# Performance work log

Measured on AMD Instinct MI355X. Metric: run time of the kernel, lower is better.

Reference implementation:

```python
import jax, jax.numpy as jnp
from jax import lax
import numpy as np

B, S, I, H, L = 128, 256, 512, 768, 2  # batch, seq, input, hidden, layers


def _lstm_dir(x_seq, Wx, bx, Wh, bh, h0, c0):
    """Run one LSTM direction over x_seq [B,S,D]. Gate order f,i,g,o (as torch.chunk)."""
    xg = jnp.einsum('bsd,dg->bsg', x_seq, Wx) + bx  # precompute input projections [B,S,4H]

    def step(carry, xg_t):
        h, c = carry
        gates = xg_t + h @ Wh + bh
        f, i, g, o = jnp.split(gates, 4, axis=-1)
        c = jax.nn.sigmoid(f) * c + jax.nn.sigmoid(i) * jnp.tanh(g)
        h = jax.nn.sigmoid(o) * jnp.tanh(c)
        return (h, c), h

    (h, c), hs = lax.scan(step, (h0, c0), jnp.swapaxes(xg, 0, 1))  # scan over time
    return jnp.swapaxes(hs, 0, 1), h, c  # outputs [B,S,H], final h, c


def _mk_params(key, in_dim, hid):
    k1, k2 = jax.random.split(key)
    s_x = 1.0 / np.sqrt(in_dim)
    s_h = 1.0 / np.sqrt(hid)
    Wx = jax.random.uniform(k1, (in_dim, 4 * hid), jnp.float32, -s_x, s_x)
    bx = jnp.zeros((4 * hid,), jnp.float32)
    Wh = jax.random.uniform(k2, (hid, 4 * hid), jnp.float32, -s_h, s_h)
    bh = jnp.zeros((4 * hid,), jnp.float32)
    return Wx, bx, Wh, bh


def setup_inputs() -> dict:
    key = jax.random.key(0)
    ks = jax.random.split(key, 5)
    x = jax.random.normal(ks[0], (B, S, I), jnp.float32)
    out = {'x': x}
    names = [('f0', I), ('f1', H), ('b0', I), ('b1', H)]
    for k, (tag, in_dim) in zip(ks[1:], names):
        Wx, bx, Wh, bh = _mk_params(k, in_dim, H)
        out[f'Wx_{tag}'] = Wx
        out[f'bx_{tag}'] = bx
        out[f'Wh_{tag}'] = Wh
        out[f'bh_{tag}'] = bh
    return out


def reference(x, Wx_f0, bx_f0, Wh_f0, bh_f0, Wx_f1, bx_f1, Wh_f1, bh_f1,
              Wx_b0, bx_b0, Wh_b0, bh_b0, Wx_b1, bx_b1, Wh_b1, bh_b1):
    b = x.shape[0]
    z = jnp.zeros((b, H), x.dtype)
    fwd_params = [(Wx_f0, bx_f0, Wh_f0, bh_f0), (Wx_f1, bx_f1, Wh_f1, bh_f1)]
    bwd_params = [(Wx_b0, bx_b0, Wh_b0, bh_b0), (Wx_b1, bx_b1, Wh_b1, bh_b1)]

    inp_f = x
    inp_b = jnp.flip(x, axis=1)  # backward direction consumes reversed sequence
    h_f, c_f, h_b, c_b = [], [], [], []
    for layer in range(L):
        inp_f, hf, cf = _lstm_dir(inp_f, *fwd_params[layer], z, z)
        h_f.append(hf); c_f.append(cf)
        inp_b, hb, cb = _lstm_dir(inp_b, *bwd_params[layer], z, z)
        h_b.append(hb); c_b.append(cb)

    output = jnp.concatenate([inp_f, jnp.flip(inp_b, axis=1)], axis=-1)  # [B,S,2H]
    h_n = jnp.stack(h_f + h_b, axis=0)  # [2L,B,H], forward layers then backward
    c_n = jnp.stack(c_f + c_b, axis=0)
    return output, h_n, c_n
```

## Files before the change

### kernel.cpp

```cpp
#include <hip/hip_runtime.h>

#define BATCH 128
#define SEQ   256
#define IDIM  512
#define HDIM  768
#define G4    3072
#define BK    32
#define LSTR  72

typedef __bf16 bf16;
typedef __bf16 bf16x8 __attribute__((ext_vector_type(8)));
typedef float  f32x4  __attribute__((ext_vector_type(4)));

__device__ __forceinline__ float sigf(float x){ return 1.f/(1.f + __expf(-x)); }
__device__ __forceinline__ float tanhf_(float x){ return 1.f - 2.f/(1.f + __expf(2.f*x)); }


__global__ void convert_x_k(const float* __restrict__ x, bf16* __restrict__ xb){
  long i = ((long)blockIdx.x*256 + threadIdx.x)*8;
  float4 a = *(const float4*)(x+i);
  float4 b = *(const float4*)(x+i+4);
  bf16x8 o;
  o[0]=(bf16)a.x; o[1]=(bf16)a.y; o[2]=(bf16)a.z; o[3]=(bf16)a.w;
  o[4]=(bf16)b.x; o[5]=(bf16)b.y; o[6]=(bf16)b.z; o[7]=(bf16)b.w;
  *(bf16x8*)(xb+i) = o;
}

__global__ void build_wt_k(const float* __restrict__ wx, const float* __restrict__ wh,
                           bf16* __restrict__ wt, int k0, int kc){
  int idx = blockIdx.x*256 + threadIdx.x;
  int c = idx / kc;
  int k = idx - c*kc;
  int g = (c >> 4) & 3;
  int j = ((c >> 6) << 4) | (c & 15);
  int oc = g*HDIM + j;
  float v = (k < k0) ? wx[(long)k*G4 + oc] : wh[(long)(k-k0)*G4 + oc];
  wt[idx] = (bf16)v;
}

__global__ void build_bias_k(const float* __restrict__ bx, const float* __restrict__ bh,
                             float* __restrict__ bc){
  int c = blockIdx.x*256 + threadIdx.x;
  int g = (c >> 4) & 3;
  int j = ((c >> 6) << 4) | (c & 15);
  int oc = g*HDIM + j;
  bc[c] = bx[oc] + bh[oc];
}


struct CellP {
  const bf16* seg0;
  const bf16* seg1;
  const bf16* wt;
  const float* bias;
  float* cbuf;
  bf16*  hout;
  float* out;
  float* hn;
  float* cn;
  int s0stride, k0, kc, active;
};
struct StepArgs { CellP cell[4]; };

__launch_bounds__(256, 2)
__global__ void lstm_step_k(StepArgs args){
  const CellP p = args.cell[blockIdx.x / 48];
  if (!p.active) return;
  int r = blockIdx.x % 48;
  int mtile = r / 24, ntile = r % 24;
  int tid = threadIdx.x;
  int lane = tid & 63, wave = tid >> 6;
  int wm = wave >> 1, wn = wave & 1;
  int l15 = lane & 15, q = lane >> 4;

  __shared__ __align__(16) bf16 lds_a[64*LSTR];
  __shared__ __align__(16) bf16 lds_b[128*LSTR];

  f32x4 acc[2][4] = {};

  int arow = tid >> 2;
  int akp  = (tid & 3) << 3;
  int brow = tid >> 1;
  int bkp  = (tid & 1) << 4;

  int ga   = mtile*64 + arow;
  int ncol = ntile*128 + brow;
  const bf16* wrow  = p.wt + (long)ncol * p.kc;
  const bf16* aseg0 = p.seg0 + (long)ga * p.s0stride;
  const bf16* aseg1 = p.seg1 + ga * HDIM;

  int nk = p.kc / BK;
  for (int kb = 0; kb < nk; ++kb){
    int k  = kb*BK;
    int ka = k + akp;
    const bf16* asrc = (ka < p.k0) ? (aseg0 + ka) : (aseg1 + (ka - p.k0));
    bf16x8 av  = *(const bf16x8*)asrc;
    bf16x8 bv0 = *(const bf16x8*)(wrow + k + bkp);
    bf16x8 bv1 = *(const bf16x8*)(wrow + k + bkp + 8);
    __syncthreads();
    *(bf16x8*)(lds_a + arow*LSTR + akp)     = av;
    *(bf16x8*)(lds_b + brow*LSTR + bkp)     = bv0;
    *(bf16x8*)(lds_b + brow*LSTR + bkp + 8) = bv1;
    __syncthreads();
    bf16x8 af[2], bfr[4];
#pragma unroll
    for (int mi=0; mi<2; ++mi)
      af[mi] = *(const bf16x8*)(lds_a + (wm*32 + mi*16 + l15)*LSTR + q*8);
#pragma unroll
    for (int ni=0; ni<4; ++ni)
      bfr[ni] = *(const bf16x8*)(lds_b + (wn*64 + ni*16 + l15)*LSTR + q*8);
#pragma unroll
    for (int mi=0; mi<2; ++mi)
#pragma unroll
      for (int ni=0; ni<4; ++ni)
        acc[mi][ni] = __builtin_amdgcn_mfma_f32_16x16x32_bf16(af[mi], bfr[ni], acc[mi][ni], 0, 0, 0);
  }

  int colb = ntile*128 + wn*64;
  int j = ((colb >> 6) << 4) | l15;
  float bias4[4];
#pragma unroll
  for (int ni=0; ni<4; ++ni) bias4[ni] = p.bias[colb + ni*16 + l15];

#pragma unroll
  for (int mi=0; mi<2; ++mi){
    int b0 = mtile*64 + wm*32 + mi*16 + q*4;
#pragma unroll
    for (int rg=0; rg<4; ++rg){
      int b = b0 + rg;
      float fg = acc[mi][0][rg] + bias4[0];
      float ig = acc[mi][1][rg] + bias4[1];
      float gg = acc[mi][2][rg] + bias4[2];
      float og = acc[mi][3][rg] + bias4[3];
      float co = p.cbuf[b*HDIM + j];
      float cn = sigf(fg)*co + sigf(ig)*tanhf_(gg);
      float h  = sigf(og)*tanhf_(cn);
      p.cbuf[b*HDIM + j] = cn;
      p.hout[b*HDIM + j] = (bf16)h;
      if (p.out) p.out[(long)b*(SEQ*2*HDIM) + j] = h;
      if (p.hn){ p.hn[b*HDIM + j] = h; p.cn[b*HDIM + j] = cn; }
    }
  }
}


extern "C" void kernel_launch(void* const* d_in, const int* in_sizes, int n_in,
                              void* d_out, int out_size, void* d_ws, size_t ws_size,
                              hipStream_t stream){
  (void)in_sizes; (void)n_in; (void)out_size; (void)ws_size;
  const float* x = (const float*)d_in[0];
  const float* Wx[4]; const float* bxp[4]; const float* Whp[4]; const float* bhp[4];
  for (int t=0; t<4; ++t){
    Wx[t]  = (const float*)d_in[1 + 4*t];
    bxp[t] = (const float*)d_in[2 + 4*t];
    Whp[t] = (const float*)d_in[3 + 4*t];
    bhp[t] = (const float*)d_in[4 + 4*t];
  }
  const int tag[4] = {0, 2, 1, 3};
  const int k0c[4] = {IDIM, IDIM, HDIM, HDIM};
  const int kcc[4] = {IDIM+HDIM, IDIM+HDIM, 2*HDIM, 2*HDIM};

  char* ws = (char*)d_ws;
  size_t off = 0;
  auto take = [&](size_t bytes)->char*{ char* pp = ws + off; off += (bytes + 255) & ~(size_t)255; return pp; };

  bf16* xb = (bf16*)take((size_t)BATCH*SEQ*IDIM*2);
  bf16* wt[4];    for (int c=0;c<4;++c) wt[c]   = (bf16*)take((size_t)G4*kcc[c]*2);
  float* bias[4]; for (int c=0;c<4;++c) bias[c] = (float*)take((size_t)G4*4);
  bf16* hseq[4];  for (int c=0;c<4;++c) hseq[c] = (bf16*)take((size_t)SEQ*BATCH*HDIM*2);
  bf16* zeros = (bf16*)take((size_t)BATCH*HDIM*2);
  float* cbuf[4]; for (int c=0;c<4;++c) cbuf[c] = (float*)take((size_t)BATCH*HDIM*4);

  size_t zlen = (size_t)BATCH*HDIM*2 + 4*(size_t)BATCH*HDIM*4;
  hipMemsetAsync(zeros, 0, zlen, stream);

  convert_x_k<<<dim3((BATCH*SEQ*IDIM)/(8*256)), dim3(256), 0, stream>>>(x, xb);
  for (int c=0;c<4;++c)
    build_wt_k<<<dim3((G4*kcc[c])/256), dim3(256), 0, stream>>>(Wx[tag[c]], Whp[tag[c]], wt[c], k0c[c], kcc[c]);
  for (int c=0;c<4;++c)
    build_bias_k<<<dim3(G4/256), dim3(256), 0, stream>>>(bxp[tag[c]], bhp[tag[c]], bias[c]);

  float* outF = (float*)d_out;
  float* hnF  = outF + (size_t)BATCH*SEQ*2*HDIM;
  float* cnF  = hnF + (size_t)4*BATCH*HDIM;
  const int hnidx[4] = {0, 2, 1, 3};
  const size_t BH = (size_t)BATCH*HDIM;

  for (int kk=0; kk<=SEQ; ++kk){
    StepArgs A;
    for (int c=0; c<2; ++c){
      CellP& P = A.cell[c];
      int t = (kk < SEQ) ? kk : 0;
      P.active = (kk < SEQ);
      int ts = (c==0) ? t : (SEQ-1-t);
      P.seg0 = xb + (size_t)ts*IDIM;
      P.s0stride = SEQ*IDIM;
      P.k0 = k0c[c]; P.kc = kcc[c];
      P.seg1 = (t==0) ? zeros : (hseq[c] + (size_t)(t-1)*BH);
      P.wt = wt[c]; P.bias = bias[c]; P.cbuf = cbuf[c];
      P.hout = hseq[c] + (size_t)t*BH;
      P.out = nullptr;
      if (P.active && t == SEQ-1){ P.hn = hnF + hnidx[c]*BH; P.cn = cnF + hnidx[c]*BH; }
      else { P.hn = nullptr; P.cn = nullptr; }
    }
    for (int c=2; c<4; ++c){
      CellP& P = A.cell[c];
      int t = (kk >= 1) ? (kk-1) : 0;
      P.active = (kk >= 1);
      P.seg0 = hseq[c-2] + (size_t)t*BH;
      P.s0stride = HDIM;
      P.k0 = k0c[c]; P.kc = kcc[c];
      P.seg1 = (t==0) ? zeros : (hseq[c] + (size_t)(t-1)*BH);
      P.wt = wt[c]; P.bias = bias[c]; P.cbuf = cbuf[c];
      P.hout = hseq[c] + (size_t)t*BH;
      P.out = (c==2) ? (outF + (size_t)t*2*HDIM)
                     : (outF + (size_t)(SEQ-1-t)*2*HDIM + HDIM);
      if (P.active && t == SEQ-1){ P.hn = hnF + hnidx[c]*BH; P.cn = cnF + hnidx[c]*BH; }
      else { P.hn = nullptr; P.cn = nullptr; }
    }
    lstm_step_k<<<dim3(192), dim3(256), 0, stream>>>(A);
  }
}
```

Baseline: 8.049 ms.

## Replace per-step launches with a persistent cooperative LSTM kernel using grid barriers

```diff
diff --git a/kernel.cpp b/kernel.cpp
--- a/kernel.cpp
+++ b/kernel.cpp
@@ -1,12 +1,16 @@
 #include <hip/hip_runtime.h>
+
 
 #define BATCH 128
 #define SEQ   256
 #define IDIM  512
 #define HDIM  768
 #define G4    3072
-#define BK    32
-#define LSTR  72
+#define NBLK  256
+#define NPHASE (SEQ + 3)
+#define WSTR  776
+#define W0STR 520
+#define HSLOT (BATCH * HDIM)
 
 typedef __bf16 bf16;
 typedef __bf16 bf16x8 __attribute__((ext_vector_type(8)));
@@ -14,6 +18,9 @@
 
 __device__ __forceinline__ float sigf(float x){ return 1.f/(1.f + __expf(-x)); }
 __device__ __forceinline__ float tanhf_(float x){ return 1.f - 2.f/(1.f + __expf(2.f*x)); }
+__device__ __forceinline__ f32x4 mfma16(bf16x8 a, bf16x8 b, f32x4 c){
+  return __builtin_amdgcn_mfma_f32_16x16x32_bf16(a, b, c, 0, 0, 0);
+}
 
 
 __global__ void convert_x_k(const float* __restrict__ x, bf16* __restrict__ xb){
@@ -26,119 +33,244 @@
   *(bf16x8*)(xb+i) = o;
 }
 
-__global__ void build_wt_k(const float* __restrict__ wx, const float* __restrict__ wh,
-                           bf16* __restrict__ wt, int k0, int kc){
+__global__ void build_wp_k(const float* __restrict__ src, bf16* __restrict__ dst, int K){
   int idx = blockIdx.x*256 + threadIdx.x;
-  int c = idx / kc;
-  int k = idx - c*kc;
-  int g = (c >> 4) & 3;
-  int j = ((c >> 6) << 4) | (c & 15);
-  int oc = g*HDIM + j;
-  float v = (k < k0) ? wx[(long)k*G4 + oc] : wh[(long)(k-k0)*G4 + oc];
-  wt[idx] = (bf16)v;
+  int c = idx / K, k = idx - c*K;
+  int oc = ((c>>4)&3)*HDIM + (((c>>6)<<4) | (c&15));
+  dst[idx] = (bf16)src[(size_t)k*G4 + oc];
 }
 
 __global__ void build_bias_k(const float* __restrict__ bx, const float* __restrict__ bh,
                              float* __restrict__ bc){
   int c = blockIdx.x*256 + threadIdx.x;
-  int g = (c >> 4) & 3;
-  int j = ((c >> 6) << 4) | (c & 15);
-  int oc = g*HDIM + j;
+  int oc = ((c>>4)&3)*HDIM + (((c>>6)<<4) | (c&15));
   bc[c] = bx[oc] + bh[oc];
 }
 
 
-struct CellP {
-  const bf16* seg0;
-  const bf16* seg1;
-  const bf16* wt;
-  const float* bias;
-  float* cbuf;
-  bf16*  hout;
-  float* out;
-  float* hn;
-  float* cn;
-  int s0stride, k0, kc, active;
+struct PA {
+  const bf16* xb;
+  const bf16* whp[4];
+  const bf16* wx1p[2];
+  const bf16* wx0p[2];
+  const float* biasp[4];
+  float* p0[2];
+  float* p1[2];
+  bf16* h0r[2];
+  bf16* h1r[2];
+  const bf16* zeros;
+  unsigned* bar;
+  float* out; float* hn; float* cn;
 };
-struct StepArgs { CellP cell[4]; };
-
-__launch_bounds__(256, 2)
-__global__ void lstm_step_k(StepArgs args){
-  const CellP p = args.cell[blockIdx.x / 48];
-  if (!p.active) return;
-  int r = blockIdx.x % 48;
-  int mtile = r / 24, ntile = r % 24;
-  int tid = threadIdx.x;
-  int lane = tid & 63, wave = tid >> 6;
-  int wm = wave >> 1, wn = wave & 1;
-  int l15 = lane & 15, q = lane >> 4;
-
-  __shared__ __align__(16) bf16 lds_a[64*LSTR];
-  __shared__ __align__(16) bf16 lds_b[128*LSTR];
-
-  f32x4 acc[2][4] = {};
-
-  int arow = tid >> 2;
-  int akp  = (tid & 3) << 3;
-  int brow = tid >> 1;
-  int bkp  = (tid & 1) << 4;
-
-  int ga   = mtile*64 + arow;
-  int ncol = ntile*128 + brow;
-  const bf16* wrow  = p.wt + (long)ncol * p.kc;
-  const bf16* aseg0 = p.seg0 + (long)ga * p.s0stride;
-  const bf16* aseg1 = p.seg1 + ga * HDIM;
-
-  int nk = p.kc / BK;
-  for (int kb = 0; kb < nk; ++kb){
-    int k  = kb*BK;
-    int ka = k + akp;
-    const bf16* asrc = (ka < p.k0) ? (aseg0 + ka) : (aseg1 + (ka - p.k0));
-    bf16x8 av  = *(const bf16x8*)asrc;
-    bf16x8 bv0 = *(const bf16x8*)(wrow + k + bkp);
-    bf16x8 bv1 = *(const bf16x8*)(wrow + k + bkp + 8);
+
+__device__ __forceinline__ void gridbar(unsigned* bar, int phase){
+  __syncthreads();
+  if (threadIdx.x == 0){
+    __threadfence();
+    __hip_atomic_fetch_add(bar, 1u, __ATOMIC_ACQ_REL, __HIP_MEMORY_SCOPE_AGENT);
+    const unsigned tgt = (unsigned)(NBLK * phase);
+    while (__hip_atomic_load(bar, __ATOMIC_ACQUIRE, __HIP_MEMORY_SCOPE_AGENT) < tgt)
+      __builtin_amdgcn_s_sleep(2);
+    __threadfence();
+  }
+  __syncthreads();
+}
+
+__launch_bounds__(256, 1)
+__global__ void lstm_persist(PA a){
+  extern __shared__ __align__(16) char smem[];
+  const int tid = threadIdx.x;
+  const int bx  = blockIdx.x;
+  const int w   = tid >> 6;
+  const int lane = tid & 63;
+  const int l15 = lane & 15, q = lane >> 4;
+
+  if (bx < 192){
+    const int role = bx / 48, g = bx - role*48;
+    const int layer = role >> 1, dir = role & 1;
+    const int colbase = g * 64;
+    bf16* wlds  = (bf16*)smem;
+    bf16* w0lds = (bf16*)(smem + 64*WSTR*2);
+    bf16* hlds  = (bf16*)(smem + 64*WSTR*2 + 32*W0STR*2) + w*512;
+
+    { const bf16* src = a.whp[role] + (size_t)colbase * HDIM;
+      for (int i = tid; i < 64*HDIM/8; i += 256){
+        int r = i/96, k8 = i - r*96;
+        *(bf16x8*)(wlds + r*WSTR + k8*8) = *(const bf16x8*)(src + (size_t)r*HDIM + k8*8);
+      }
+      const int chunk0 = g + layer*48;
+      const bf16* s0 = a.wx0p[dir] + (size_t)chunk0 * (32*IDIM);
+      for (int i = tid; i < 32*IDIM/8; i += 256){
+        int r = i/64, k8 = i - r*64;
+        *(bf16x8*)(w0lds + r*W0STR + k8*8) = *(const bf16x8*)(s0 + (size_t)r*IDIM + k8*8);
+      }
+    }
     __syncthreads();
-    *(bf16x8*)(lds_a + arow*LSTR + akp)     = av;
-    *(bf16x8*)(lds_b + brow*LSTR + bkp)     = bv0;
-    *(bf16x8*)(lds_b + brow*LSTR + bkp + 8) = bv1;
+
+    float bias4[4];
+#pragma unroll
+    for (int n=0;n<4;++n) bias4[n] = a.biasp[role][colbase + n*16 + l15];
+    float cst[8];
+#pragma unroll
+    for (int i=0;i<8;++i) cst[i] = 0.f;
+
+    bf16* hr = layer ? a.h1r[dir] : a.h0r[dir];
+    float* pring = layer ? a.p1[dir] : a.p0[dir];
+    float* p0out = a.p0[dir];
+    const int c0 = (g + layer*48) * 32;
+    const int hnidx = layer + dir*2;
+    const int row_lo = w*32 + l15;
+    const int rb = w*32 + q*4;
+
+    for (int kk = 0; kk < NPHASE; ++kk){
+      if (kk) gridbar(a.bar, kk);
+
+      const int t = kk - (layer ? 3 : 1);
+      if (t >= 0 && t < SEQ){
+        const bf16* hprev = (t == 0) ? a.zeros : (hr + (size_t)((t-1)&1) * HSLOT);
+        const bf16* ar0 = hprev + (size_t)row_lo * HDIM + q*8;
+        const bf16* ar1 = ar0 + 16*HDIM;
+        f32x4 acc[2][4];
+#pragma unroll
+        for (int m=0;m<2;++m)
+#pragma unroll
+          for (int n=0;n<4;++n) acc[m][n] = (f32x4){0.f,0.f,0.f,0.f};
+
+        bf16x8 a0 = *(const bf16x8*)(ar0);
+        bf16x8 a1 = *(const bf16x8*)(ar1);
+        for (int ks = 0; ks < 24; ++ks){
+          const int kn = ks < 23 ? ks+1 : 23;
+          bf16x8 n0 = *(const bf16x8*)(ar0 + kn*32);
+          bf16x8 n1 = *(const bf16x8*)(ar1 + kn*32);
+          const bf16* wb = wlds + ks*32 + q*8;
+#pragma unroll
+          for (int n=0;n<4;++n){
+            bf16x8 bv = *(const bf16x8*)(wb + (n*16 + l15)*WSTR);
+            acc[0][n] = mfma16(a0, bv, acc[0][n]);
+            acc[1][n] = mfma16(a1, bv, acc[1][n]);
+          }
+          a0 = n0; a1 = n1;
+        }
+
+        const float* pin = pring + (size_t)(t&1) * (G4*BATCH);
+        bf16* hout = hr + (size_t)(t&1) * HSLOT;
+        const int tout = dir ? (SEQ-1-t) : t;
+#pragma unroll
+        for (int m=0;m<2;++m){
+          const int r0 = rb + m*16;
+          f32x4 pv[4];
+#pragma unroll
+          for (int n=0;n<4;++n)
+            pv[n] = *(const f32x4*)(pin + (size_t)(colbase + n*16 + l15)*BATCH + r0);
+#pragma unroll
+          for (int r=0;r<4;++r){
+            const int b = r0 + r;
+            float fg = acc[m][0][r] + pv[0][r] + bias4[0];
+            float ig = acc[m][1][r] + pv[1][r] + bias4[1];
+            float gg = acc[m][2][r] + pv[2][r] + bias4[2];
+            float og = acc[m][3][r] + pv[3][r] + bias4[3];
+            float c  = sigf(fg)*cst[m*4+r] + sigf(ig)*tanhf_(gg);
+            float h  = sigf(og)*tanhf_(c);
+            cst[m*4+r] = c;
+            hlds[(m*16 + q*4 + r)*16 + l15] = (bf16)h;
+            if (layer)
+              a.out[(size_t)b*(SEQ*2*HDIM) + (size_t)tout*(2*HDIM) + dir*HDIM + g*16 + l15] = h;
+            if (t == SEQ-1){
+              a.hn[(size_t)hnidx*HSLOT + (size_t)b*HDIM + g*16 + l15] = h;
+              a.cn[(size_t)hnidx*HSLOT + (size_t)b*HDIM + g*16 + l15] = c;
+            }
+          }
+        }
+        __syncthreads();
+        { const int hrow = w*32 + (lane>>1);
+          const int half = lane & 1;
+          bf16x8 hv = *(const bf16x8*)(hlds + (lane>>1)*16 + half*8);
+          *(bf16x8*)(hout + (size_t)hrow*HDIM + g*16 + half*8) = hv;
+        }
+      }
+
+      if (kk < SEQ){
+        const int t0 = kk;
+        const int ts = dir ? (SEQ-1-t0) : t0;
+        const bf16* xr0 = a.xb + (size_t)row_lo*(SEQ*IDIM) + (size_t)ts*IDIM + q*8;
+        const bf16* xr1 = xr0 + (size_t)16*(SEQ*IDIM);
+        f32x4 acc0[2][2];
+#pragma unroll
+        for (int m=0;m<2;++m)
+#pragma unroll
+          for (int n=0;n<2;++n) acc0[m][n] = (f32x4){0.f,0.f,0.f,0.f};
+        bf16x8 a0 = *(const bf16x8*)(xr0);
+        bf16x8 a1 = *(const bf16x8*)(xr1);
+        for (int ks = 0; ks < 16; ++ks){
+          const int kn = ks < 15 ? ks+1 : 15;
+          bf16x8 n0 = *(const bf16x8*)(xr0 + kn*32);
+          bf16x8 n1 = *(const bf16x8*)(xr1 + kn*32);
+          const bf16* wb = w0lds + ks*32 + q*8;
+#pragma unroll
+          for (int n=0;n<2;++n){
+            bf16x8 bv = *(const bf16x8*)(wb + (n*16 + l15)*W0STR);
+            acc0[0][n] = mfma16(a0, bv, acc0[0][n]);
+            acc0[1][n] = mfma16(a1, bv, acc0[1][n]);
+          }
+          a0 = n0; a1 = n1;
+        }
+        float* pout = p0out + (size_t)(t0&1)*(G4*BATCH);
+#pragma unroll
+        for (int m=0;m<2;++m)
+#pragma unroll
+          for (int n=0;n<2;++n)
+            *(f32x4*)(pout + (size_t)(c0 + n*16 + l15)*BATCH + rb + m*16) = acc0[m][n];
+      }
+    }
+  } else {
+    const int dir = (bx - 192) >> 5, ii = (bx - 192) & 31;
+    const int c0 = ii * 96;
+    bf16* wlds = (bf16*)smem;
+    { const bf16* src = a.wx1p[dir] + (size_t)c0 * HDIM;
+      for (int i = tid; i < 96*HDIM/8; i += 256){
+        int r = i/96, k8 = i - r*96;
+        *(bf16x8*)(wlds + r*WSTR + k8*8) = *(const bf16x8*)(src + (size_t)r*HDIM + k8*8);
+      }
+    }
     __syncthreads();
-    bf16x8 af[2], bfr[4];
-#pragma unroll
-    for (int mi=0; mi<2; ++mi)
-      af[mi] = *(const bf16x8*)(lds_a + (wm*32 + mi*16 + l15)*LSTR + q*8);
-#pragma unroll
-    for (int ni=0; ni<4; ++ni)
-      bfr[ni] = *(const bf16x8*)(lds_b + (wn*64 + ni*16 + l15)*LSTR + q*8);
-#pragma unroll
-    for (int mi=0; mi<2; ++mi)
-#pragma unroll
-      for (int ni=0; ni<4; ++ni)
-        acc[mi][ni] = __builtin_amdgcn_mfma_f32_16x16x32_bf16(af[mi], bfr[ni], acc[mi][ni], 0, 0, 0);
-  }
-
-  int colb = ntile*128 + wn*64;
-  int j = ((colb >> 6) << 4) | l15;
-  float bias4[4];
-#pragma unroll
-  for (int ni=0; ni<4; ++ni) bias4[ni] = p.bias[colb + ni*16 + l15];
-
-#pragma unroll
-  for (int mi=0; mi<2; ++mi){
-    int b0 = mtile*64 + wm*32 + mi*16 + q*4;
-#pragma unroll
-    for (int rg=0; rg<4; ++rg){
-      int b = b0 + rg;
-      float fg = acc[mi][0][rg] + bias4[0];
-      float ig = acc[mi][1][rg] + bias4[1];
-      float gg = acc[mi][2][rg] + bias4[2];
-      float og = acc[mi][3][rg] + bias4[3];
-      float co = p.cbuf[b*HDIM + j];
-      float cn = sigf(fg)*co + sigf(ig)*tanhf_(gg);
-      float h  = sigf(og)*tanhf_(cn);
-      p.cbuf[b*HDIM + j] = cn;
-      p.hout[b*HDIM + j] = (bf16)h;
-      if (p.out) p.out[(long)b*(SEQ*2*HDIM) + j] = h;
-      if (p.hn){ p.hn[b*HDIM + j] = h; p.cn[b*HDIM + j] = cn; }
+    const bf16* hbase = a.h0r[dir];
+    float* pbase = a.p1[dir];
+    const int row_lo = w*32 + l15, rb = w*32 + q*4;
+
+    for (int kk = 0; kk < NPHASE; ++kk){
+      if (kk) gridbar(a.bar, kk);
+      const int t = kk - 2;
+      if (t >= 0 && t < SEQ){
+        const bf16* hp = hbase + (size_t)(t&1)*HSLOT;
+        const bf16* ar0 = hp + (size_t)row_lo*HDIM + q*8;
+        const bf16* ar1 = ar0 + 16*HDIM;
+        f32x4 acc[2][6];
+#pragma unroll
+        for (int m=0;m<2;++m)
+#pragma unroll
+          for (int n=0;n<6;++n) acc[m][n] = (f32x4){0.f,0.f,0.f,0.f};
+        bf16x8 a0 = *(const bf16x8*)(ar0);
+        bf16x8 a1 = *(const bf16x8*)(ar1);
+        for (int ks = 0; ks < 24; ++ks){
+          const int kn = ks < 23 ? ks+1 : 23;
+          bf16x8 n0 = *(const bf16x8*)(ar0 + kn*32);
+          bf16x8 n1 = *(const bf16x8*)(ar1 + kn*32);
+          const bf16* wb = wlds + ks*32 + q*8;
+#pragma unroll
+          for (int n=0;n<6;++n){
+            bf16x8 bv = *(const bf16x8*)(wb + (n*16 + l15)*WSTR);
+            acc[0][n] = mfma16(a0, bv, acc[0][n]);
+            acc[1][n] = mfma16(a1, bv, acc[1][n]);
+          }
+          a0 = n0; a1 = n1;
+        }
+        float* pout = pbase + (size_t)(t&1)*(G4*BATCH);
+#pragma unroll
+        for (int m=0;m<2;++m)
+#pragma unroll
+          for (int n=0;n<6;++n)
+            *(f32x4*)(pout + (size_t)(c0 + n*16 + l15)*BATCH + rb + m*16) = acc[m][n];
+      }
     }
   }
 }
@@ -156,68 +288,45 @@
     Whp[t] = (const float*)d_in[3 + 4*t];
     bhp[t] = (const float*)d_in[4 + 4*t];
   }
-  const int tag[4] = {0, 2, 1, 3};
-  const int k0c[4] = {IDIM, IDIM, HDIM, HDIM};
-  const int kcc[4] = {IDIM+HDIM, IDIM+HDIM, 2*HDIM, 2*HDIM};
+  const int roletag[4] = {0, 2, 1, 3};
 
   char* ws = (char*)d_ws;
   size_t off = 0;
-  auto take = [&](size_t bytes)->char*{ char* pp = ws + off; off += (bytes + 255) & ~(size_t)255; return pp; };
+  auto take = [&](size_t bytes)->char*{ char* p = ws + off; off += (bytes + 255) & ~(size_t)255; return p; };
 
   bf16* xb = (bf16*)take((size_t)BATCH*SEQ*IDIM*2);
-  bf16* wt[4];    for (int c=0;c<4;++c) wt[c]   = (bf16*)take((size_t)G4*kcc[c]*2);
-  float* bias[4]; for (int c=0;c<4;++c) bias[c] = (float*)take((size_t)G4*4);
-  bf16* hseq[4];  for (int c=0;c<4;++c) hseq[c] = (bf16*)take((size_t)SEQ*BATCH*HDIM*2);
+  PA a;
+  a.xb = xb;
+  bf16* whp_w[4]; for (int r=0;r<4;++r){ whp_w[r] = (bf16*)take((size_t)G4*HDIM*2); a.whp[r] = whp_w[r]; }
+  bf16* wx1_w[2]; for (int d=0;d<2;++d){ wx1_w[d] = (bf16*)take((size_t)G4*HDIM*2); a.wx1p[d] = wx1_w[d]; }
+  bf16* wx0_w[2]; for (int d=0;d<2;++d){ wx0_w[d] = (bf16*)take((size_t)G4*IDIM*2); a.wx0p[d] = wx0_w[d]; }
+  float* bias_w[4]; for (int r=0;r<4;++r){ bias_w[r] = (float*)take((size_t)G4*4); a.biasp[r] = bias_w[r]; }
+  for (int d=0;d<2;++d) a.p0[d] = (float*)take((size_t)2*G4*BATCH*4);
+  for (int d=0;d<2;++d) a.p1[d] = (float*)take((size_t)2*G4*BATCH*4);
+  for (int d=0;d<2;++d) a.h0r[d] = (bf16*)take((size_t)2*BATCH*HDIM*2);
+  for (int d=0;d<2;++d) a.h1r[d] = (bf16*)take((size_t)2*BATCH*HDIM*2);
   bf16* zeros = (bf16*)take((size_t)BATCH*HDIM*2);
-  float* cbuf[4]; for (int c=0;c<4;++c) cbuf[c] = (float*)take((size_t)BATCH*HDIM*4);
-
-  size_t zlen = (size_t)BATCH*HDIM*2 + 4*(size_t)BATCH*HDIM*4;
-  hipMemsetAsync(zeros, 0, zlen, stream);
+  a.zeros = zeros;
+  a.bar = (unsigned*)take(256);
+
+  hipMemsetAsync(zeros, 0, (size_t)BATCH*HDIM*2 + 256, stream);
 
   convert_x_k<<<dim3((BATCH*SEQ*IDIM)/(8*256)), dim3(256), 0, stream>>>(x, xb);
-  for (int c=0;c<4;++c)
-    build_wt_k<<<dim3((G4*kcc[c])/256), dim3(256), 0, stream>>>(Wx[tag[c]], Whp[tag[c]], wt[c], k0c[c], kcc[c]);
-  for (int c=0;c<4;++c)
-    build_bias_k<<<dim3(G4/256), dim3(256), 0, stream>>>(bxp[tag[c]], bhp[tag[c]], bias[c]);
-
-  float* outF = (float*)d_out;
-  float* hnF  = outF + (size_t)BATCH*SEQ*2*HDIM;
-  float* cnF  = hnF + (size_t)4*BATCH*HDIM;
-  const int hnidx[4] = {0, 2, 1, 3};
-  const size_t BH = (size_t)BATCH*HDIM;
-
-  for (int kk=0; kk<=SEQ; ++kk){
-    StepArgs A;
-    for (int c=0; c<2; ++c){
-      CellP& P = A.cell[c];
-      int t = (kk < SEQ) ? kk : 0;
-      P.active = (kk < SEQ);
-      int ts = (c==0) ? t : (SEQ-1-t);
-      P.seg0 = xb + (size_t)ts*IDIM;
-      P.s0stride = SEQ*IDIM;
-      P.k0 = k0c[c]; P.kc = kcc[c];
-      P.seg1 = (t==0) ? zeros : (hseq[c] + (size_t)(t-1)*BH);
-      P.wt = wt[c]; P.bias = bias[c]; P.cbuf = cbuf[c];
-      P.hout = hseq[c] + (size_t)t*BH;
-      P.out = nullptr;
-      if (P.active && t == SEQ-1){ P.hn = hnF + hnidx[c]*BH; P.cn = cnF + hnidx[c]*BH; }
-      else { P.hn = nullptr; P.cn = nullptr; }
-    }
-    for (int c=2; c<4; ++c){
-      CellP& P = A.cell[c];
-      int t = (kk >= 1) ? (kk-1) : 0;
-      P.active = (kk >= 1);
-      P.seg0 = hseq[c-2] + (size_t)t*BH;
-      P.s0stride = HDIM;
-      P.k0 = k0c[c]; P.kc = kcc[c];
-      P.seg1 = (t==0) ? zeros : (hseq[c] + (size_t)(t-1)*BH);
-      P.wt = wt[c]; P.bias = bias[c]; P.cbuf = cbuf[c];
-      P.hout = hseq[c] + (size_t)t*BH;
-      P.out = (c==2) ? (outF + (size_t)t*2*HDIM)
-                     : (outF + (size_t)(SEQ-1-t)*2*HDIM + HDIM);
-      if (P.active && t == SEQ-1){ P.hn = hnF + hnidx[c]*BH; P.cn = cnF + hnidx[c]*BH; }
-      else { P.hn = nullptr; P.cn = nullptr; }
-    }
-    lstm_step_k<<<dim3(192), dim3(256), 0, stream>>>(A);
-  }
-}
+  for (int r=0;r<4;++r)
+    build_wp_k<<<dim3(G4*HDIM/256), dim3(256), 0, stream>>>(Whp[roletag[r]], whp_w[r], HDIM);
+  build_wp_k<<<dim3(G4*HDIM/256), dim3(256), 0, stream>>>(Wx[1], wx1_w[0], HDIM);
+  build_wp_k<<<dim3(G4*HDIM/256), dim3(256), 0, stream>>>(Wx[3], wx1_w[1], HDIM);
+  build_wp_k<<<dim3(G4*IDIM/256), dim3(256), 0, stream>>>(Wx[0], wx0_w[0], IDIM);
+  build_wp_k<<<dim3(G4*IDIM/256), dim3(256), 0, stream>>>(Wx[2], wx0_w[1], IDIM);
+  for (int r=0;r<4;++r)
+    build_bias_k<<<dim3(G4/256), dim3(256), 0, stream>>>(bxp[roletag[r]], bhp[roletag[r]], bias_w[r]);
+
+  a.out = (float*)d_out;
+  a.hn  = a.out + (size_t)BATCH*SEQ*2*HDIM;
+  a.cn  = a.hn + (size_t)4*BATCH*HDIM;
+
+  const unsigned smem_bytes = 96*WSTR*2;
+  hipFuncSetAttribute((const void*)lstm_persist, hipFuncAttributeMaxDynamicSharedMemorySize, smem_bytes);
+  void* kargs[] = { &a };
+  hipLaunchCooperativeKernel((void*)lstm_persist, dim3(NBLK), dim3(256), kargs, smem_bytes, stream);
+}
```

New measurement: 14.44 ms. 1.79x slower.
